# Optimization experiments

Hardware: AMD Instinct MI355X
Metric: run time of the kernel (lower is better)

The kernel has to match this reference:

```python
import jax, jax.numpy as jnp
import numpy as np

N = 100000
E = 640000
D = 128      # node_dim == edge_dim
H = 256      # conv MLP hidden dim
EPS = 1e-5


def _ln(x, g, b):
    mu = jnp.mean(x, axis=-1, keepdims=True)
    var = jnp.var(x, axis=-1, keepdims=True)
    return (x - mu) * jax.lax.rsqrt(var + EPS) * g + b


def _conv_mlp(x, W1, b1, g1, be1, W2, b2, g2, be2):
    h = _ln(x @ W1 + b1, g1, be1)          # (N, H)
    h = jax.nn.relu(h)
    return _ln(h @ W2 + b2, g2, be2)        # (N, D)


def setup_inputs() -> dict:
    key = jax.random.key(0)
    ks = jax.random.split(key, 6)
    s1 = 1.0 / np.sqrt(D)
    s2 = 1.0 / np.sqrt(H)
    return {
        "x": jax.random.normal(ks[0], (N, D), dtype=jnp.float32),
        "edge_index": jax.random.randint(ks[1], (2, E), 0, N, dtype=jnp.int32),
        "edge_attr": jax.random.normal(ks[2], (E, D), dtype=jnp.float32),
        "W1": jax.random.uniform(ks[3], (D, H), jnp.float32, -s1, s1),
        "b1": jnp.zeros((H,), jnp.float32),
        "g1": jnp.ones((H,), jnp.float32),
        "be1": jnp.zeros((H,), jnp.float32),
        "W2": jax.random.uniform(ks[4], (H, D), jnp.float32, -s2, s2),
        "b2": jnp.zeros((D,), jnp.float32),
        "g2": jnp.ones((D,), jnp.float32),
        "be2": jnp.zeros((D,), jnp.float32),
        "g_out": jnp.ones((D,), jnp.float32),
        "b_out": jnp.zeros((D,), jnp.float32),
    }


def reference(x, edge_index, edge_attr, W1, b1, g1, be1, W2, b2, g2, be2, g_out, b_out):
    # Conv(h[w]) for all nodes once, then gather per edge (vectorized form of
    # the per-node/per-neighbor loops in the torch module).
    conv = _conv_mlp(x, W1, b1, g1, be1, W2, b2, g2, be2)   # (N, D)
    src, dst = edge_index[0], edge_index[1]
    msgs = conv[dst] * edge_attr                            # (E, D): Conv(h[w]) * e[v,w]
    agg = jax.ops.segment_sum(msgs, src, num_segments=N)    # scatter-add into v
    return _ln(agg + x, g_out, b_out)
```

## Files before the change

### kernel.cpp

```cpp
#include <hip/hip_runtime.h>

constexpr int D = 128;
constexpr int H = 256;
constexpr float EPS = 1e-5f;

typedef __attribute__((ext_vector_type(8))) __bf16  bf16x8;
typedef __attribute__((ext_vector_type(4))) float   f32x4;

static __device__ __forceinline__ unsigned short f2bfu(float f) {
    unsigned u = __float_as_uint(f);
    return (unsigned short)((u + 0x7FFFu + ((u >> 16) & 1u)) >> 16);
}
static __device__ __forceinline__ float bf2f(unsigned short u) {
    return __uint_as_float((unsigned)u << 16);
}

static __device__ __forceinline__ f32x4 mfma16x16x32(bf16x8 a, bf16x8 b, f32x4 c) {
    return __builtin_amdgcn_mfma_f32_16x16x32_bf16(a, b, c, 0, 0, 0);
}

static __device__ __forceinline__ void pack_w_elem(
    const float* __restrict__ W, unsigned short* __restrict__ Wp, int K, int Ncols, int e)
{
    int i  = e & 7;
    int l  = (e >> 3) & 63;
    int jt = e >> 9;
    int nt = K >> 5;
    int j  = jt / nt;
    int t  = jt - j * nt;
    int k  = 32 * t + ((l >> 4) << 3) + i;
    int c  = 16 * j + (l & 15);
    Wp[e] = f2bfu(W[(size_t)k * Ncols + c]);
}

__global__ __launch_bounds__(256) void prep_kernel(
    const float* __restrict__ W1, unsigned short* __restrict__ W1p,
    const float* __restrict__ W2, unsigned short* __restrict__ W2p,
    int* __restrict__ counts, int N)
{
    int b = blockIdx.x;
    if (b < 128) {
        pack_w_elem(W1, W1p, D, H, b * 256 + threadIdx.x);
    } else if (b < 256) {
        pack_w_elem(W2, W2p, H, D, (b - 128) * 256 + threadIdx.x);
    } else {
        int i = (b - 256) * 256 + threadIdx.x;
        if (i < N) counts[i] = 0;
    }
}

__global__ __launch_bounds__(256) void conv_hist_kernel(
    const float* __restrict__ x,
    const unsigned short* __restrict__ W1p, const float* __restrict__ b1,
    const float* __restrict__ g1, const float* __restrict__ be1,
    const unsigned short* __restrict__ W2p, const float* __restrict__ b2,
    const float* __restrict__ g2, const float* __restrict__ be2,
    unsigned short* __restrict__ convb, int N,
    const int* __restrict__ eidx, int* __restrict__ counts, int E, int convBlocks)
{
    __shared__ unsigned short Hs[64 * 256];
    __shared__ unsigned short Ws[2][8192];

    if ((int)blockIdx.x >= convBlocks) {
        int e = (blockIdx.x - convBlocks) * 256 + threadIdx.x;
        if (e < E) atomicAdd(&counts[eidx[e]], 1);
        return;
    }

    const int wv   = threadIdx.x >> 6;
    const int lane = threadIdx.x & 63;
    const int rrow = lane & 15;
    const int kgrp = lane >> 4;
    const int r0   = blockIdx.x * 64 + wv * 16;

    float4 sv0, sv1, sv2, sv3;
    auto issueW = [&](const unsigned short* Wp, int c) {
        const float4* s = (const float4*)(Wp + c * 8192);
        sv0 = s[threadIdx.x];
        sv1 = s[threadIdx.x + 256];
        sv2 = s[threadIdx.x + 512];
        sv3 = s[threadIdx.x + 768];
    };
    auto writeS = [&](int b) {
        float4* d = (float4*)Ws[b];
        d[threadIdx.x]       = sv0;
        d[threadIdx.x + 256] = sv1;
        d[threadIdx.x + 512] = sv2;
        d[threadIdx.x + 768] = sv3;
    };

    int arow = r0 + rrow; if (arow >= N) arow = N - 1;
    const float* xr = x + (size_t)arow * D + kgrp * 8;
    bf16x8 A1[4];
    #pragma unroll
    for (int t = 0; t < 4; ++t) {
        float4 fa = *(const float4*)(xr + t * 32);
        float4 fb = *(const float4*)(xr + t * 32 + 4);
        bf16x8 a;
        a[0] = (__bf16)fa.x; a[1] = (__bf16)fa.y; a[2] = (__bf16)fa.z; a[3] = (__bf16)fa.w;
        a[4] = (__bf16)fb.x; a[5] = (__bf16)fb.y; a[6] = (__bf16)fb.z; a[7] = (__bf16)fb.w;
        A1[t] = a;
    }

    f32x4 acc[16];
    #pragma unroll
    for (int j = 0; j < 16; ++j) acc[j] = (f32x4){0.f, 0.f, 0.f, 0.f};

    issueW(W1p, 0); writeS(0); __syncthreads();
    #pragma unroll
    for (int c = 0; c < 4; ++c) {
        if (c < 3) issueW(W1p, c + 1);
        #pragma unroll
        for (int jj = 0; jj < 4; ++jj) {
            #pragma unroll
            for (int t = 0; t < 4; ++t) {
                bf16x8 B = *(const bf16x8*)((const char*)Ws[c & 1]
                             + ((jj * 4 + t) * 512 + lane * 8) * 2);
                acc[c * 4 + jj] = mfma16x16x32(A1[t], B, acc[c * 4 + jj]);
            }
        }
        if (c < 3) writeS((c + 1) & 1);
        __syncthreads();
    }

    float b1r[16], g1r[16], be1r[16];
    #pragma unroll
    for (int j = 0; j < 16; ++j) {
        int c = 16 * j + rrow;
        b1r[j] = b1[c]; g1r[j] = g1[c]; be1r[j] = be1[c];
    }

    float s1[4] = {0,0,0,0}, s2[4] = {0,0,0,0};
    #pragma unroll
    for (int j = 0; j < 16; ++j) {
        #pragma unroll
        for (int r = 0; r < 4; ++r) {
            float v = acc[j][r] + b1r[j];
            acc[j][r] = v;
            s1[r] += v; s2[r] += v * v;
        }
    }
    #pragma unroll
    for (int m = 1; m < 16; m <<= 1) {
        #pragma unroll
        for (int r = 0; r < 4; ++r) {
            s1[r] += __shfl_xor(s1[r], m);
            s2[r] += __shfl_xor(s2[r], m);
        }
    }

    issueW(W2p, 0);

    #pragma unroll
    for (int r = 0; r < 4; ++r) {
        float mu  = s1[r] * (1.f / H);
        float var = s2[r] * (1.f / H) - mu * mu;
        float rs  = rsqrtf(var + EPS);
        int row = wv * 16 + kgrp * 4 + r;
        #pragma unroll
        for (int j = 0; j < 16; ++j) {
            float h = fmaxf((acc[j][r] - mu) * rs * g1r[j] + be1r[j], 0.f);
            int byte = (row << 9) + ((16 * j + rrow) << 1);
            byte ^= (row & 15) << 4;
            *(unsigned short*)((char*)Hs + byte) = f2bfu(h);
        }
    }

    bf16x8 A2[8];
    #pragma unroll
    for (int t = 0; t < 8; ++t) {
        int row  = wv * 16 + rrow;
        int byte = (row << 9) + ((t * 32 + kgrp * 8) << 1);
        byte ^= (row & 15) << 4;
        A2[t] = *(const bf16x8*)((const char*)Hs + byte);
    }

    writeS(0); __syncthreads();

    f32x4 acc2[8];
    #pragma unroll
    for (int j = 0; j < 8; ++j) acc2[j] = (f32x4){0.f, 0.f, 0.f, 0.f};
    #pragma unroll
    for (int c = 0; c < 4; ++c) {
        if (c < 3) issueW(W2p, c + 1);
        #pragma unroll
        for (int jj = 0; jj < 2; ++jj) {
            #pragma unroll
            for (int t = 0; t < 8; ++t) {
                bf16x8 B = *(const bf16x8*)((const char*)Ws[c & 1]
                             + ((jj * 8 + t) * 512 + lane * 8) * 2);
                acc2[c * 2 + jj] = mfma16x16x32(A2[t], B, acc2[c * 2 + jj]);
            }
        }
        if (c < 3) writeS((c + 1) & 1);
        __syncthreads();
    }

    float b2r[8], g2r[8], be2r[8];
    #pragma unroll
    for (int j = 0; j < 8; ++j) {
        int c = 16 * j + rrow;
        b2r[j] = b2[c]; g2r[j] = g2[c]; be2r[j] = be2[c];
    }

    float u1[4] = {0,0,0,0}, u2[4] = {0,0,0,0};
    #pragma unroll
    for (int j = 0; j < 8; ++j) {
        #pragma unroll
        for (int r = 0; r < 4; ++r) {
            float v = acc2[j][r] + b2r[j];
            acc2[j][r] = v;
            u1[r] += v; u2[r] += v * v;
        }
    }
    #pragma unroll
    for (int m = 1; m < 16; m <<= 1) {
        #pragma unroll
        for (int r = 0; r < 4; ++r) {
            u1[r] += __shfl_xor(u1[r], m);
            u2[r] += __shfl_xor(u2[r], m);
        }
    }
    #pragma unroll
    for (int r = 0; r < 4; ++r) {
        float mu  = u1[r] * (1.f / D);
        float var = u2[r] * (1.f / D) - mu * mu;
        float rs  = rsqrtf(var + EPS);
        int grow = r0 + kgrp * 4 + r;
        if (grow < N) {
            #pragma unroll
            for (int j = 0; j < 8; ++j) {
                float o = (acc2[j][r] - mu) * rs * g2r[j] + be2r[j];
                convb[(size_t)grow * D + 16 * j + rrow] = f2bfu(o);
            }
        }
    }
}

__global__ __launch_bounds__(256) void scan1_kernel(
    const int* __restrict__ counts, int* __restrict__ row_start,
    int* __restrict__ bsums, int N)
{
    __shared__ int sd[256];
    int t  = threadIdx.x;
    int i0 = blockIdx.x * 1024 + t * 4;
    int c0 = (i0+0 < N) ? counts[i0+0] : 0;
    int c1 = (i0+1 < N) ? counts[i0+1] : 0;
    int c2 = (i0+2 < N) ? counts[i0+2] : 0;
    int c3 = (i0+3 < N) ? counts[i0+3] : 0;
    int s  = c0 + c1 + c2 + c3;
    sd[t] = s;
    __syncthreads();
    #pragma unroll
    for (int off = 1; off < 256; off <<= 1) {
        int v = (t >= off) ? sd[t - off] : 0;
        __syncthreads();
        sd[t] += v;
        __syncthreads();
    }
    int ex = sd[t] - s;
    if (i0+0 < N) row_start[i0+0] = ex;
    if (i0+1 < N) row_start[i0+1] = ex + c0;
    if (i0+2 < N) row_start[i0+2] = ex + c0 + c1;
    if (i0+3 < N) row_start[i0+3] = ex + c0 + c1 + c2;
    if (t == 255) bsums[blockIdx.x] = sd[255];
}

__global__ __launch_bounds__(128) void scan2_kernel(int* __restrict__ bsums, int NB)
{
    __shared__ int sd[128];
    int t = threadIdx.x;
    int v = (t < NB) ? bsums[t] : 0;
    sd[t] = v;
    __syncthreads();
    #pragma unroll
    for (int off = 1; off < 128; off <<= 1) {
        int u = (t >= off) ? sd[t - off] : 0;
        __syncthreads();
        sd[t] += u;
        __syncthreads();
    }
    if (t < NB) bsums[t] = sd[t] - v;
}

__global__ __launch_bounds__(256) void scan3_kernel(
    int* __restrict__ row_start, const int* __restrict__ bsums,
    int* __restrict__ cursor, int N)
{
    int i = blockIdx.x * blockDim.x + threadIdx.x;
    if (i < N) {
        int r = row_start[i] + bsums[i >> 10];
        row_start[i] = r;
        cursor[i]    = r;
    }
}

__global__ __launch_bounds__(256) void fill_kernel(
    const int* __restrict__ eidx, int* __restrict__ cursor,
    int2* __restrict__ edat, int E)
{
    int e = blockIdx.x * blockDim.x + threadIdx.x;
    if (e < E) {
        int s = eidx[e];
        int p = atomicAdd(&cursor[s], 1);
        edat[p] = make_int2(e, eidx[E + e]);
    }
}

__global__ __launch_bounds__(256) void gather_ln_kernel(
    const float* __restrict__ x, const unsigned short* __restrict__ convb,
    const float* __restrict__ eattr,
    const int* __restrict__ row_start, const int2* __restrict__ edat,
    const float* __restrict__ g, const float* __restrict__ b,
    float* __restrict__ out, int N, int E)
{
    int node = blockIdx.x * 4 + (threadIdx.x >> 6);
    if (node >= N) return;
    int lane = threadIdx.x & 63;
    int half = lane >> 5;
    int c4   = (lane & 31) * 4;

    float4 acc = make_float4(0.f, 0.f, 0.f, 0.f);
    int je = (node + 1 < N) ? row_start[node + 1] : E;
    int j  = row_start[node] + half;

    for (; j + 2 < je; j += 4) {
        int2 ea = edat[j];
        int2 eb = edat[j + 2];
        ushort4 ca = *(const ushort4*)(convb + (size_t)ea.y * D + c4);
        float4  aa = *(const float4*) (eattr + (size_t)ea.x * D + c4);
        ushort4 cb = *(const ushort4*)(convb + (size_t)eb.y * D + c4);
        float4  ab = *(const float4*) (eattr + (size_t)eb.x * D + c4);
        acc.x += bf2f(ca.x) * aa.x; acc.y += bf2f(ca.y) * aa.y;
        acc.z += bf2f(ca.z) * aa.z; acc.w += bf2f(ca.w) * aa.w;
        acc.x += bf2f(cb.x) * ab.x; acc.y += bf2f(cb.y) * ab.y;
        acc.z += bf2f(cb.z) * ab.z; acc.w += bf2f(cb.w) * ab.w;
    }
    if (j < je) {
        int2 ea = edat[j];
        ushort4 ca = *(const ushort4*)(convb + (size_t)ea.y * D + c4);
        float4  aa = *(const float4*) (eattr + (size_t)ea.x * D + c4);
        acc.x += bf2f(ca.x) * aa.x; acc.y += bf2f(ca.y) * aa.y;
        acc.z += bf2f(ca.z) * aa.z; acc.w += bf2f(ca.w) * aa.w;
    }

    if (half == 0) {
        float4 xv = *(const float4*)(x + (size_t)node * D + c4);
        acc.x += xv.x; acc.y += xv.y; acc.z += xv.z; acc.w += xv.w;
    }
    acc.x += __shfl_xor(acc.x, 32);
    acc.y += __shfl_xor(acc.y, 32);
    acc.z += __shfl_xor(acc.z, 32);
    acc.w += __shfl_xor(acc.w, 32);

    float s1 = acc.x + acc.y + acc.z + acc.w;
    float s2 = acc.x*acc.x + acc.y*acc.y + acc.z*acc.z + acc.w*acc.w;
    #pragma unroll
    for (int o = 1; o < 32; o <<= 1) {
        s1 += __shfl_xor(s1, o);
        s2 += __shfl_xor(s2, o);
    }
    float mu  = s1 * (1.f / D);
    float var = s2 * (1.f / D) - mu * mu;
    float rs  = rsqrtf(var + EPS);
    if (half == 0) {
        float4 gv = *(const float4*)(g + c4);
        float4 bv = *(const float4*)(b + c4);
        float4 o4;
        o4.x = (acc.x - mu) * rs * gv.x + bv.x;
        o4.y = (acc.y - mu) * rs * gv.y + bv.y;
        o4.z = (acc.z - mu) * rs * gv.z + bv.z;
        o4.w = (acc.w - mu) * rs * gv.w + bv.w;
        *(float4*)(out + (size_t)node * D + c4) = o4;
    }
}

extern "C" void kernel_launch(void* const* d_in, const int* in_sizes, int n_in,
                              void* d_out, int out_size, void* d_ws, size_t ws_size,
                              hipStream_t stream) {
    const float* x     = (const float*)d_in[0];
    const int*   eidx  = (const int*)  d_in[1];
    const float* eattr = (const float*)d_in[2];
    const float* W1    = (const float*)d_in[3];
    const float* b1    = (const float*)d_in[4];
    const float* g1    = (const float*)d_in[5];
    const float* be1   = (const float*)d_in[6];
    const float* W2    = (const float*)d_in[7];
    const float* b2    = (const float*)d_in[8];
    const float* g2    = (const float*)d_in[9];
    const float* be2   = (const float*)d_in[10];
    const float* g_out = (const float*)d_in[11];
    const float* b_out = (const float*)d_in[12];

    const int N = in_sizes[0] / D;
    const int E = in_sizes[1] / 2;

    float* out = (float*)d_out;

    auto align_up = [](size_t v) { return (v + 255) & ~(size_t)255; };
    size_t convB = align_up((size_t)N * D * sizeof(unsigned short));
    size_t cntB  = align_up((size_t)N * sizeof(int));
    size_t rsB   = align_up((size_t)N * sizeof(int));
    size_t bsB   = align_up(128 * sizeof(int));
    size_t edB   = align_up((size_t)E * sizeof(int2));
    size_t w1B   = align_up((size_t)D * H * sizeof(unsigned short));

    char* w = (char*)d_ws;
    unsigned short* convb     = (unsigned short*)(w);
    int*            counts    = (int*)(w + convB);
    int*            row_start = (int*)(w + convB + cntB);
    int*            bsums     = (int*)(w + convB + cntB + rsB);
    int2*           edat      = (int2*)(w + convB + cntB + rsB + bsB);
    unsigned short* W1p       = (unsigned short*)(w + convB + cntB + rsB + bsB + edB);
    unsigned short* W2p       = (unsigned short*)(w + convB + cntB + rsB + bsB + edB + w1B);

    int zeroBlocks = (N + 255) / 256;
    prep_kernel<<<256 + zeroBlocks, 256, 0, stream>>>(W1, W1p, W2, W2p, counts, N);

    int convBlocks = (N + 63) / 64;
    int histBlocks = (E + 255) / 256;
    conv_hist_kernel<<<convBlocks + histBlocks, 256, 0, stream>>>(
        x, W1p, b1, g1, be1, W2p, b2, g2, be2, convb, N, eidx, counts, E, convBlocks);

    int NB = (N + 1023) / 1024;
    scan1_kernel<<<NB, 256, 0, stream>>>(counts, row_start, bsums, N);
    scan2_kernel<<<1, 128, 0, stream>>>(bsums, NB);
    scan3_kernel<<<(N + 255) / 256, 256, 0, stream>>>(row_start, bsums, counts, N);

    fill_kernel<<<(E + 255) / 256, 256, 0, stream>>>(eidx, counts, edat, E);

    gather_ln_kernel<<<(N + 3) / 4, 256, 0, stream>>>(
        x, convb, eattr, row_start, edat, g_out, b_out, out, N, E);
}
```

Baseline: 211.2 us.

## Coalesce conv output stores via LDS and fuse scan into decoupled lookback

Conv MLP results are first written to swizzled shared memory, then copied to global memory as 16-byte vector stores per row instead of scattered 2-byte stores. The three-kernel prefix scan is replaced by a single-pass decoupled-lookback scan that also initialises the cursors. The flags it needs are zeroed in the prep kernel. This removes two launches and an extra pass over row_start, but adds inter-block spin-waiting and extra shared-memory traffic.

After: 240.5 us. +13.9%, slower.

```diff
diff --git a/kernel.cpp b/kernel.cpp
--- a/kernel.cpp
+++ b/kernel.cpp
@@ -36,16 +36,18 @@
 __global__ __launch_bounds__(256) void prep_kernel(
     const float* __restrict__ W1, unsigned short* __restrict__ W1p,
     const float* __restrict__ W2, unsigned short* __restrict__ W2p,
-    int* __restrict__ counts, int N)
+    int* __restrict__ counts, int* __restrict__ flags, int N, int zeroBlocks)
 {
     int b = blockIdx.x;
     if (b < 128) {
         pack_w_elem(W1, W1p, D, H, b * 256 + threadIdx.x);
     } else if (b < 256) {
         pack_w_elem(W2, W2p, H, D, (b - 128) * 256 + threadIdx.x);
-    } else {
+    } else if (b < 256 + zeroBlocks) {
         int i = (b - 256) * 256 + threadIdx.x;
         if (i < N) counts[i] = 0;
+    } else {
+        if (threadIdx.x < 128) flags[threadIdx.x] = 0;
     }
 }
 
@@ -221,29 +223,47 @@
             u2[r] += __shfl_xor(u2[r], m);
         }
     }
+
     #pragma unroll
     for (int r = 0; r < 4; ++r) {
         float mu  = u1[r] * (1.f / D);
         float var = u2[r] * (1.f / D) - mu * mu;
         float rs  = rsqrtf(var + EPS);
-        int grow = r0 + kgrp * 4 + r;
+        int row = wv * 16 + kgrp * 4 + r;
+        #pragma unroll
+        for (int j = 0; j < 8; ++j) {
+            float o = (acc2[j][r] - mu) * rs * g2r[j] + be2r[j];
+            int byte = (row << 9) + ((16 * j + rrow) << 1);
+            byte ^= (row & 15) << 4;
+            *(unsigned short*)((char*)Hs + byte) = f2bfu(o);
+        }
+    }
+
+    {
+        int lrow = wv * 16 + (lane >> 2);
+        int grow = r0 + (lane >> 2);
         if (grow < N) {
             #pragma unroll
-            for (int j = 0; j < 8; ++j) {
-                float o = (acc2[j][r] - mu) * rs * g2r[j] + be2r[j];
-                convb[(size_t)grow * D + 16 * j + rrow] = f2bfu(o);
+            for (int k = 0; k < 4; ++k) {
+                int chunk = (lane & 3) * 4 + k;
+                int byte  = (lrow << 9) + (chunk << 4);
+                byte ^= (lrow & 15) << 4;
+                uint4 v = *(const uint4*)((const char*)Hs + byte);
+                *(uint4*)(convb + (size_t)grow * D + chunk * 8) = v;
             }
         }
     }
 }
 
-__global__ __launch_bounds__(256) void scan1_kernel(
+__global__ __launch_bounds__(256) void scan_lb_kernel(
     const int* __restrict__ counts, int* __restrict__ row_start,
-    int* __restrict__ bsums, int N)
+    int* __restrict__ cursor,
+    int* __restrict__ agg, int* __restrict__ incl, int* __restrict__ flags, int N)
 {
     __shared__ int sd[256];
-    int t  = threadIdx.x;
-    int i0 = blockIdx.x * 1024 + t * 4;
+    __shared__ int sexc;
+    int b = blockIdx.x, t = threadIdx.x;
+    int i0 = b * 1024 + t * 4;
     int c0 = (i0+0 < N) ? counts[i0+0] : 0;
     int c1 = (i0+1 < N) ? counts[i0+1] : 0;
     int c2 = (i0+2 < N) ? counts[i0+2] : 0;
@@ -258,41 +278,41 @@
         sd[t] += v;
         __syncthreads();
     }
-    int ex = sd[t] - s;
-    if (i0+0 < N) row_start[i0+0] = ex;
-    if (i0+1 < N) row_start[i0+1] = ex + c0;
-    if (i0+2 < N) row_start[i0+2] = ex + c0 + c1;
-    if (i0+3 < N) row_start[i0+3] = ex + c0 + c1 + c2;
-    if (t == 255) bsums[blockIdx.x] = sd[255];
-}
-
-__global__ __launch_bounds__(128) void scan2_kernel(int* __restrict__ bsums, int NB)
-{
-    __shared__ int sd[128];
-    int t = threadIdx.x;
-    int v = (t < NB) ? bsums[t] : 0;
-    sd[t] = v;
+    int ex    = sd[t] - s;
+    int total = sd[255];
+
+    if (t == 0) {
+        if (b == 0) {
+            __hip_atomic_store(&incl[0], total, __ATOMIC_RELEASE, __HIP_MEMORY_SCOPE_AGENT);
+            __hip_atomic_store(&flags[0], 2, __ATOMIC_RELEASE, __HIP_MEMORY_SCOPE_AGENT);
+            sexc = 0;
+        } else {
+            __hip_atomic_store(&agg[b], total, __ATOMIC_RELEASE, __HIP_MEMORY_SCOPE_AGENT);
+            __hip_atomic_store(&flags[b], 1, __ATOMIC_RELEASE, __HIP_MEMORY_SCOPE_AGENT);
+            int exc = 0;
+            for (int j = b - 1; j >= 0; ) {
+                int f;
+                do {
+                    f = __hip_atomic_load(&flags[j], __ATOMIC_ACQUIRE, __HIP_MEMORY_SCOPE_AGENT);
+                } while (f == 0);
+                if (f == 2) {
+                    exc += __hip_atomic_load(&incl[j], __ATOMIC_ACQUIRE, __HIP_MEMORY_SCOPE_AGENT);
+                    break;
+                }
+                exc += __hip_atomic_load(&agg[j], __ATOMIC_ACQUIRE, __HIP_MEMORY_SCOPE_AGENT);
+                --j;
+            }
+            __hip_atomic_store(&incl[b], exc + total, __ATOMIC_RELEASE, __HIP_MEMORY_SCOPE_AGENT);
+            __hip_atomic_store(&flags[b], 2, __ATOMIC_RELEASE, __HIP_MEMORY_SCOPE_AGENT);
+            sexc = exc;
+        }
+    }
     __syncthreads();
-    #pragma unroll
-    for (int off = 1; off < 128; off <<= 1) {
-        int u = (t >= off) ? sd[t - off] : 0;
-        __syncthreads();
-        sd[t] += u;
-        __syncthreads();
-    }
-    if (t < NB) bsums[t] = sd[t] - v;
-}
-
-__global__ __launch_bounds__(256) void scan3_kernel(
-    int* __restrict__ row_start, const int* __restrict__ bsums,
-    int* __restrict__ cursor, int N)
-{
-    int i = blockIdx.x * blockDim.x + threadIdx.x;
-    if (i < N) {
-        int r = row_start[i] + bsums[i >> 10];
-        row_start[i] = r;
-        cursor[i]    = r;
-    }
+    int base = sexc + ex;
+    if (i0+0 < N) { row_start[i0+0] = base;              cursor[i0+0] = base; }
+    if (i0+1 < N) { row_start[i0+1] = base + c0;         cursor[i0+1] = base + c0; }
+    if (i0+2 < N) { row_start[i0+2] = base + c0 + c1;    cursor[i0+2] = base + c0 + c1; }
+    if (i0+3 < N) { row_start[i0+3] = base + c0 + c1 + c2; cursor[i0+3] = base + c0 + c1 + c2; }
 }
 
 __global__ __launch_bounds__(256) void fill_kernel(
@@ -409,13 +429,16 @@
     unsigned short* convb     = (unsigned short*)(w);
     int*            counts    = (int*)(w + convB);
     int*            row_start = (int*)(w + convB + cntB);
-    int*            bsums     = (int*)(w + convB + cntB + rsB);
-    int2*           edat      = (int2*)(w + convB + cntB + rsB + bsB);
-    unsigned short* W1p       = (unsigned short*)(w + convB + cntB + rsB + bsB + edB);
-    unsigned short* W2p       = (unsigned short*)(w + convB + cntB + rsB + bsB + edB + w1B);
+    int*            flags     = (int*)(w + convB + cntB + rsB);
+    int*            agg       = (int*)(w + convB + cntB + rsB + bsB);
+    int*            incl      = (int*)(w + convB + cntB + rsB + 2*bsB);
+    int2*           edat      = (int2*)(w + convB + cntB + rsB + 3*bsB);
+    unsigned short* W1p       = (unsigned short*)(w + convB + cntB + rsB + 3*bsB + edB);
+    unsigned short* W2p       = (unsigned short*)(w + convB + cntB + rsB + 3*bsB + edB + w1B);
 
     int zeroBlocks = (N + 255) / 256;
-    prep_kernel<<<256 + zeroBlocks, 256, 0, stream>>>(W1, W1p, W2, W2p, counts, N);
+    prep_kernel<<<256 + zeroBlocks + 1, 256, 0, stream>>>(
+        W1, W1p, W2, W2p, counts, flags, N, zeroBlocks);
 
     int convBlocks = (N + 63) / 64;
     int histBlocks = (E + 255) / 256;
@@ -423,9 +446,7 @@
         x, W1p, b1, g1, be1, W2p, b2, g2, be2, convb, N, eidx, counts, E, convBlocks);
 
     int NB = (N + 1023) / 1024;
-    scan1_kernel<<<NB, 256, 0, stream>>>(counts, row_start, bsums, N);
-    scan2_kernel<<<1, 128, 0, stream>>>(bsums, NB);
-    scan3_kernel<<<(N + 255) / 256, 256, 0, stream>>>(row_start, bsums, counts, N);
+    scan_lb_kernel<<<NB, 256, 0, stream>>>(counts, row_start, counts, agg, incl, flags, N);
 
     fill_kernel<<<(E + 255) / 256, 256, 0, stream>>>(eidx, counts, edat, E);
 
```
